# Kernel tuning notes

Hardware: AMD Instinct MI355X
Metric: run time of the kernel (lower is better)

The kernel has to match this reference:

```python
import jax, jax.numpy as jnp
import numpy as np

E = 512       # embed_dim
H = 8         # num_heads
DH = E // H   # head dim
F = 2048      # dim_feedforward
KS = 33       # NATTEN kernel_size (dilation=1)
NCLS = 1
B = 2
L = 4096      # local tokens (total seq = L + NCLS)
EPS = 1e-5


def layernorm(x, g, b):
    mu = jnp.mean(x, axis=-1, keepdims=True)
    var = jnp.mean(jnp.square(x - mu), axis=-1, keepdims=True)
    return (x - mu) * jax.lax.rsqrt(var + EPS) * g + b


def natten_1d(x, qkv_w, qkv_b, proj_w, proj_b):
    # Neighborhood attention 1D, dilation=1, non-causal, no rel-pos bias.
    b, l, e = x.shape
    qkv = x @ qkv_w.T + qkv_b                       # [b, l, 3E]
    q, k, v = jnp.split(qkv, 3, axis=-1)
    q = q.reshape(b, l, H, DH) * (DH ** -0.5)
    k = k.reshape(b, l, H, DH)
    v = v.reshape(b, l, H, DH)
    # NATTEN window: centered, shifted at edges to keep exactly KS in-bounds neighbors
    starts = jnp.clip(jnp.arange(l) - KS // 2, 0, l - KS)   # [l]
    idx = starts[:, None] + jnp.arange(KS)                  # [l, KS]
    kn = k[:, idx]                                          # [b, l, KS, H, DH]
    vn = v[:, idx]                                          # [b, l, KS, H, DH]
    attn = jnp.einsum('blhd,blkhd->bhlk', q, kn)
    attn = jax.nn.softmax(attn, axis=-1)
    out = jnp.einsum('bhlk,blkhd->blhd', attn, vn).reshape(b, l, e)
    return out @ proj_w.T + proj_b


def global_mha(q_in, kv_in, in_w, in_b, out_w, out_b):
    # torch nn.MultiheadAttention, batch_first, no masks
    bq, lq, e = q_in.shape
    lk = kv_in.shape[1]
    wq, wk, wv = jnp.split(in_w, 3, axis=0)
    bqp, bkp, bvp = jnp.split(in_b, 3, axis=0)
    q = (q_in @ wq.T + bqp).reshape(bq, lq, H, DH) * (DH ** -0.5)
    k = (kv_in @ wk.T + bkp).reshape(bq, lk, H, DH)
    v = (kv_in @ wv.T + bvp).reshape(bq, lk, H, DH)
    attn = jax.nn.softmax(jnp.einsum('bqhd,bkhd->bhqk', q, k), axis=-1)
    out = jnp.einsum('bhqk,bkhd->bqhd', attn, v).reshape(bq, lq, e)
    return out @ out_w.T + out_b


def setup_inputs() -> dict:
    key = jax.random.key(0)
    ks = jax.random.split(key, 16)
    s = 0.02
    return {
        'x': jax.random.normal(ks[0], (B, L + NCLS, E), jnp.float32),
        'ln1_g': jnp.ones((E,), jnp.float32),
        'ln1_b': jnp.zeros((E,), jnp.float32),
        'qkv_w': jax.random.normal(ks[1], (3 * E, E), jnp.float32) * s,
        'qkv_b': jnp.zeros((3 * E,), jnp.float32),
        'na_proj_w': jax.random.normal(ks[2], (E, E), jnp.float32) * s,
        'na_proj_b': jnp.zeros((E,), jnp.float32),
        'in_proj_w': jax.random.normal(ks[3], (3 * E, E), jnp.float32) * s,
        'in_proj_b': jnp.zeros((3 * E,), jnp.float32),
        'out_w': jax.random.normal(ks[4], (E, E), jnp.float32) * s,
        'out_b': jnp.zeros((E,), jnp.float32),
        'ln2_g': jnp.ones((E,), jnp.float32),
        'ln2_b': jnp.zeros((E,), jnp.float32),
        'fc1_w': jax.random.normal(ks[5], (F, E), jnp.float32) * s,
        'fc1_b': jnp.zeros((F,), jnp.float32),
        'fc2_w': jax.random.normal(ks[6], (E, F), jnp.float32) * s,
        'fc2_b': jnp.zeros((E,), jnp.float32),
    }


def reference(x, ln1_g, ln1_b, qkv_w, qkv_b, na_proj_w, na_proj_b,
              in_proj_w, in_proj_b, out_w, out_b, ln2_g, ln2_b,
              fc1_w, fc1_b, fc2_w, fc2_b):
    res = x
    xn = layernorm(x, ln1_g, ln1_b)
    x_local = natten_1d(xn[:, :-NCLS, :], qkv_w, qkv_b, na_proj_w, na_proj_b)
    tmp_key = jnp.concatenate([x_local, xn[:, -NCLS:, :]], axis=1)
    x_cls = global_mha(xn[:, -NCLS:, :], tmp_key, in_proj_w, in_proj_b, out_w, out_b)
    x = res + jnp.concatenate([x_local, x_cls], axis=1)
    res = x
    xn = layernorm(x, ln2_g, ln2_b)
    h = jax.nn.silu(xn @ fc1_w.T + fc1_b)
    return res + (h @ fc2_w.T + fc2_b)
```

## Files before the change

### kernel.cpp

```cpp
#include <hip/hip_runtime.h>
#include <hip/hip_bf16.h>
#include <cstdint>
#include <cstddef>

#define E    512
#define H    8
#define DHD  64
#define FDIM 2048
#define KS   33
#define BB   2
#define LL   4096
#define LP1  4097
#define NTOK 8194
#define NLOC 8192

typedef unsigned short ushort_t;
typedef __bf16 bf16x8_t __attribute__((ext_vector_type(8)));
typedef float  f32x4_t  __attribute__((ext_vector_type(4)));

__device__ __forceinline__ float b2f(unsigned short h) {
  union { unsigned int u; float f; } un; un.u = ((unsigned int)h) << 16; return un.f;
}
__device__ __forceinline__ unsigned short f2b(float f) {
  union { float f; unsigned int u; } un; un.f = f;
  unsigned int u = un.u;
  return (unsigned short)((u + 0x7FFFu + ((u >> 16) & 1u)) >> 16);
}

__device__ __forceinline__ void gload16(const ushort_t* g, ushort_t* l) {
  __builtin_amdgcn_global_load_lds(
      (const __attribute__((address_space(1))) void*)g,
      (__attribute__((address_space(3))) void*)l,
      16, 0, 0);
}

#define BM 128

template<int BNT, int ACT, int OUTF, int ADDRES, int INRM, int OUTRM, int PARTIAL>
__global__ __launch_bounds__(256) void gemm_bt(
    const ushort_t* __restrict__ A, const ushort_t* __restrict__ W,
    const float* __restrict__ bias, float* __restrict__ outF,
    ushort_t* __restrict__ outB, const float* __restrict__ res,
    int M, int N, int K, int klen)
{
  constexpr int NFRAG = BNT / 32;
  __shared__ ushort_t Alds[BM * 64];
  __shared__ ushort_t Blds[BNT * 64];
  const int t    = threadIdx.x;
  const int lane = t & 63;
  const int w    = t >> 6;
  const int wr   = w >> 1, wc = w & 1;
  const int bmBase = blockIdx.x * BM;
  const int bnBase = blockIdx.y * BNT;
  const int z    = blockIdx.z;
  const int kbeg = z * klen;

  f32x4_t zero = {0.f, 0.f, 0.f, 0.f};
  f32x4_t acc[4][NFRAG];
  #pragma unroll
  for (int m = 0; m < 4; ++m)
    #pragma unroll
    for (int n = 0; n < NFRAG; ++n) acc[m][n] = zero;

  const int srow = t >> 3;
  const int jsw8 = ((t & 7) ^ (srow & 7)) * 8;
  int arow[4];
  #pragma unroll
  for (int r = 0; r < 4; ++r) {
    int rr = bmBase + r * 32 + srow;
    if (INRM) rr += rr >> 12;
    else if (rr >= M) rr = M - 1;
    arow[r] = rr;
  }
  int brow[NFRAG];
  #pragma unroll
  for (int r = 0; r < NFRAG; ++r) brow[r] = bnBase + r * 32 + srow;

  const int frow = lane & 15;
  const int g    = lane >> 4;

  for (int k0 = kbeg; k0 < kbeg + klen; k0 += 64) {
    #pragma unroll
    for (int r = 0; r < 4; ++r)
      gload16(A + (size_t)arow[r] * K + k0 + jsw8, &Alds[(size_t)(r * 256 + t) * 8]);
    #pragma unroll
    for (int r = 0; r < NFRAG; ++r)
      gload16(W + (size_t)brow[r] * K + k0 + jsw8, &Blds[(size_t)(r * 256 + t) * 8]);
    __syncthreads();
    #pragma unroll
    for (int kk2 = 0; kk2 < 2; ++kk2) {
      bf16x8_t af[4], bfv[NFRAG];
      const int kosw = ((kk2 * 4 + g) ^ (frow & 7)) << 4;
      #pragma unroll
      for (int m = 0; m < 4; ++m) {
        int row = wr * 64 + m * 16 + frow;
        af[m] = *reinterpret_cast<const bf16x8_t*>((char*)Alds + row * 128 + kosw);
      }
      #pragma unroll
      for (int n = 0; n < NFRAG; ++n) {
        int row = wc * (BNT / 2) + n * 16 + frow;
        bfv[n] = *reinterpret_cast<const bf16x8_t*>((char*)Blds + row * 128 + kosw);
      }
      #pragma unroll
      for (int m = 0; m < 4; ++m)
        #pragma unroll
        for (int n = 0; n < NFRAG; ++n)
          acc[m][n] = __builtin_amdgcn_mfma_f32_16x16x32_bf16(af[m], bfv[n], acc[m][n], 0, 0, 0);
    }
    __syncthreads();
  }

  const int rbase = g * 4;
  const int cbase = frow;
  float* po = nullptr;
  if (PARTIAL) po = (z == 0) ? outF : (float*)outB;
  #pragma unroll
  for (int m = 0; m < 4; ++m) {
    #pragma unroll
    for (int r = 0; r < 4; ++r) {
      int gr = bmBase + wr * 64 + m * 16 + rbase + r;
      if (gr < M) {
        int orow = OUTRM ? gr + (gr >> 12) : gr;
        #pragma unroll
        for (int n = 0; n < NFRAG; ++n) {
          int gc = bnBase + wc * (BNT / 2) + n * 16 + cbase;
          float v = acc[m][n][r];
          if (PARTIAL) {
            po[(size_t)orow * N + gc] = v;
          } else {
            v += bias[gc];
            if (ACT == 1) v = v / (1.f + __expf(-v));
            if (ADDRES) v += res[(size_t)gr * N + gc];
            if (OUTF) outF[(size_t)orow * N + gc] = v;
            else      outB[(size_t)orow * N + gc] = f2b(v);
          }
        }
      }
    }
  }
}

__global__ __launch_bounds__(256) void fc2_reduce(
    float* __restrict__ out, const float* __restrict__ p0,
    const float* __restrict__ bias, const float* __restrict__ xa)
{
  size_t i = (size_t)blockIdx.x * 256 + threadIdx.x;
  float4 o = reinterpret_cast<const float4*>(out)[i];
  float4 a = reinterpret_cast<const float4*>(p0)[i];
  float4 x = reinterpret_cast<const float4*>(xa)[i];
  float4 bcol = reinterpret_cast<const float4*>(bias)[i & 127];
  o.x += a.x + x.x + bcol.x;
  o.y += a.y + x.y + bcol.y;
  o.z += a.z + x.z + bcol.z;
  o.w += a.w + x.w + bcol.w;
  reinterpret_cast<float4*>(out)[i] = o;
}

__global__ __launch_bounds__(256) void ln_fused1(
    const float* __restrict__ x, const float* __restrict__ g,
    const float* __restrict__ be, ushort_t* __restrict__ xn,
    ushort_t* __restrict__ tmpk)
{
  __shared__ float sh[4];
  const int row = blockIdx.x;
  const int t = threadIdx.x;
  const float* xr = x + (size_t)row * E;
  float v0 = xr[t], v1 = xr[t + 256];
  float sum = v0 + v1;
  #pragma unroll
  for (int o = 32; o; o >>= 1) sum += __shfl_xor(sum, o);
  if ((t & 63) == 0) sh[t >> 6] = sum;
  __syncthreads();
  float mean = (sh[0] + sh[1] + sh[2] + sh[3]) * (1.f / E);
  __syncthreads();
  float d0 = v0 - mean, d1 = v1 - mean;
  float vs = d0 * d0 + d1 * d1;
  #pragma unroll
  for (int o = 32; o; o >>= 1) vs += __shfl_xor(vs, o);
  if ((t & 63) == 0) sh[t >> 6] = vs;
  __syncthreads();
  float var = (sh[0] + sh[1] + sh[2] + sh[3]) * (1.f / E);
  float rstd = rsqrtf(var + 1e-5f);
  unsigned short o0 = f2b(d0 * rstd * g[t] + be[t]);
  unsigned short o1 = f2b(d1 * rstd * g[t + 256] + be[t + 256]);
  xn[(size_t)row * E + t] = o0;
  xn[(size_t)row * E + t + 256] = o1;
  if ((row % LP1) == LL) {
    tmpk[(size_t)row * E + t] = o0;
    tmpk[(size_t)row * E + t + 256] = o1;
  }
}

__global__ __launch_bounds__(256) void resid_ln2(
    const float* __restrict__ x, const ushort_t* __restrict__ tmpk,
    const float* __restrict__ xcls, const float* __restrict__ g,
    const float* __restrict__ be, float* __restrict__ xa,
    ushort_t* __restrict__ xn2)
{
  __shared__ float sh[4];
  const int row = blockIdx.x;
  const int b = row / LP1, l = row % LP1;
  const int t = threadIdx.x;
  float a0, a1;
  if (l < LL) { a0 = b2f(tmpk[(size_t)row * E + t]); a1 = b2f(tmpk[(size_t)row * E + t + 256]); }
  else        { a0 = xcls[b * E + t];                a1 = xcls[b * E + t + 256]; }
  float v0 = x[(size_t)row * E + t] + a0;
  float v1 = x[(size_t)row * E + t + 256] + a1;
  xa[(size_t)row * E + t] = v0;
  xa[(size_t)row * E + t + 256] = v1;
  float sum = v0 + v1;
  #pragma unroll
  for (int o = 32; o; o >>= 1) sum += __shfl_xor(sum, o);
  if ((t & 63) == 0) sh[t >> 6] = sum;
  __syncthreads();
  float mean = (sh[0] + sh[1] + sh[2] + sh[3]) * (1.f / E);
  __syncthreads();
  float d0 = v0 - mean, d1 = v1 - mean;
  float vs = d0 * d0 + d1 * d1;
  #pragma unroll
  for (int o = 32; o; o >>= 1) vs += __shfl_xor(vs, o);
  if ((t & 63) == 0) sh[t >> 6] = vs;
  __syncthreads();
  float var = (sh[0] + sh[1] + sh[2] + sh[3]) * (1.f / E);
  float rstd = rsqrtf(var + 1e-5f);
  xn2[(size_t)row * E + t]       = f2b(d0 * rstd * g[t] + be[t]);
  xn2[(size_t)row * E + t + 256] = f2b(d1 * rstd * g[t + 256] + be[t + 256]);
}

__global__ __launch_bounds__(256) void natten_mfma(
    const ushort_t* __restrict__ qkv, ushort_t* __restrict__ out)
{
  __shared__ ushort_t KP[4][64 * 64];
  __shared__ ushort_t VT[4][64 * 72];
  const int w    = threadIdx.x >> 6;
  const int lane = threadIdx.x & 63;
  const int task = blockIdx.x * 4 + w;
  const int h  = task & 7;
  const int qb = (task >> 3) & 127;
  const int b  = task >> 10;
  const int l0 = qb * 32;
  const int kb = l0 - 16;
  const ushort_t* base = qkv + (size_t)b * LL * (3 * E);
  ushort_t* Klds = KP[w];
  ushort_t* Vt   = VT[w];

  {
    const int rsub = lane >> 3;
    const int d0   = (lane & 7) * 8;
    #pragma unroll
    for (int i = 0; i < 8; ++i) {
      int row = i * 8 + rsub;
      int gl = kb + row; gl = gl < 0 ? 0 : (gl > LL - 1 ? LL - 1 : gl);
      bf16x8_t kv = *reinterpret_cast<const bf16x8_t*>(
          base + (size_t)gl * (3 * E) + E + h * 64 + d0);
      int ba = (row * 128 + d0 * 2) ^ ((row & 7) << 4);
      *reinterpret_cast<bf16x8_t*>((char*)Klds + ba) = kv;
    }
  }
  {
    const int a  = lane & 7;
    const int c8 = lane >> 3;
    unsigned int* Vt32 = (unsigned int*)Vt;
    #pragma unroll
    for (int i = 0; i < 4; ++i) {
      int rp = i * 8 + c8;
      int g0 = kb + rp * 2;     g0 = g0 < 0 ? 0 : (g0 > LL - 1 ? LL - 1 : g0);
      int g1 = kb + rp * 2 + 1; g1 = g1 < 0 ? 0 : (g1 > LL - 1 ? LL - 1 : g1);
      const ushort_t* v0 = base + (size_t)g0 * (3 * E) + 2 * E + h * 64 + a * 8;
      const ushort_t* v1 = base + (size_t)g1 * (3 * E) + 2 * E + h * 64 + a * 8;
      ushort4 x0 = *(const ushort4*)v0,       x1 = *(const ushort4*)v1;
      ushort4 y0 = *(const ushort4*)(v0 + 4), y1 = *(const ushort4*)(v1 + 4);
      int d = a * 8;
      Vt32[(d + 0) * 36 + rp] = (unsigned)x0.x | ((unsigned)x1.x << 16);
      Vt32[(d + 1) * 36 + rp] = (unsigned)x0.y | ((unsigned)x1.y << 16);
      Vt32[(d + 2) * 36 + rp] = (unsigned)x0.z | ((unsigned)x1.z << 16);
      Vt32[(d + 3) * 36 + rp] = (unsigned)x0.w | ((unsigned)x1.w << 16);
      Vt32[(d + 4) * 36 + rp] = (unsigned)y0.x | ((unsigned)y1.x << 16);
      Vt32[(d + 5) * 36 + rp] = (unsigned)y0.y | ((unsigned)y1.y << 16);
      Vt32[(d + 6) * 36 + rp] = (unsigned)y0.z | ((unsigned)y1.z << 16);
      Vt32[(d + 7) * 36 + rp] = (unsigned)y0.w | ((unsigned)y1.w << 16);
    }
  }

  const int p = lane & 15, g = lane >> 4;
  bf16x8_t qf[2][2];
  #pragma unroll
  for (int mt = 0; mt < 2; ++mt)
    #pragma unroll
    for (int ks = 0; ks < 2; ++ks)
      qf[mt][ks] = *reinterpret_cast<const bf16x8_t*>(
          base + (size_t)(l0 + mt * 16 + p) * (3 * E) + h * 64 + ks * 32 + g * 8);

  f32x4_t zero = {0.f, 0.f, 0.f, 0.f};
  f32x4_t accS[2][4];
  #pragma unroll
  for (int mt = 0; mt < 2; ++mt)
    #pragma unroll
    for (int nt = 0; nt < 4; ++nt) accS[mt][nt] = zero;
  #pragma unroll
  for (int ks = 0; ks < 2; ++ks) {
    bf16x8_t kf[4];
    #pragma unroll
    for (int nt = 0; nt < 4; ++nt) {
      int row = nt * 16 + p;
      int ba = (row * 128 + (ks * 32 + g * 8) * 2) ^ ((row & 7) << 4);
      kf[nt] = *reinterpret_cast<const bf16x8_t*>((char*)Klds + ba);
    }
    #pragma unroll
    for (int mt = 0; mt < 2; ++mt)
      #pragma unroll
      for (int nt = 0; nt < 4; ++nt)
        accS[mt][nt] = __builtin_amdgcn_mfma_f32_16x16x32_bf16(qf[mt][ks], kf[nt], accS[mt][nt], 0, 0, 0);
  }

  ushort_t* Plds = Klds;
  #pragma unroll
  for (int mt = 0; mt < 2; ++mt) {
    #pragma unroll
    for (int r = 0; r < 4; ++r) {
      int lq = l0 + mt * 16 + g * 4 + r;
      int st = lq - 16; st = st < 0 ? 0 : (st > LL - KS ? LL - KS : st);
      int clo = st - kb, chi = clo + 32;
      float sv[4];
      float mx = -1e30f;
      #pragma unroll
      for (int nt = 0; nt < 4; ++nt) {
        int c = nt * 16 + p;
        float s = accS[mt][nt][r] * 0.125f;
        s = (c >= clo && c <= chi) ? s : -1e30f;
        sv[nt] = s;
        mx = fmaxf(mx, s);
      }
      mx = fmaxf(mx, __shfl_xor(mx, 1));
      mx = fmaxf(mx, __shfl_xor(mx, 2));
      mx = fmaxf(mx, __shfl_xor(mx, 4));
      mx = fmaxf(mx, __shfl_xor(mx, 8));
      float sum = 0.f;
      #pragma unroll
      for (int nt = 0; nt < 4; ++nt) { float e = __expf(sv[nt] - mx); sv[nt] = e; sum += e; }
      sum += __shfl_xor(sum, 1);
      sum += __shfl_xor(sum, 2);
      sum += __shfl_xor(sum, 4);
      sum += __shfl_xor(sum, 8);
      float inv = 1.f / sum;
      int q = mt * 16 + g * 4 + r;
      #pragma unroll
      for (int nt = 0; nt < 4; ++nt)
        Plds[q * 72 + nt * 16 + p] = f2b(sv[nt] * inv);
    }
  }

  f32x4_t accO[2][4];
  #pragma unroll
  for (int mt = 0; mt < 2; ++mt)
    #pragma unroll
    for (int nt = 0; nt < 4; ++nt) accO[mt][nt] = zero;
  #pragma unroll
  for (int ks = 0; ks < 2; ++ks) {
    bf16x8_t pf[2], vf[4];
    #pragma unroll
    for (int mt = 0; mt < 2; ++mt)
      pf[mt] = *reinterpret_cast<const bf16x8_t*>(
          (char*)Plds + (mt * 16 + p) * 144 + (ks * 32 + g * 8) * 2);
    #pragma unroll
    for (int nt = 0; nt < 4; ++nt)
      vf[nt] = *reinterpret_cast<const bf16x8_t*>(
          (char*)Vt + (nt * 16 + p) * 144 + (ks * 32 + g * 8) * 2);
    #pragma unroll
    for (int mt = 0; mt < 2; ++mt)
      #pragma unroll
      for (int nt = 0; nt < 4; ++nt)
        accO[mt][nt] = __builtin_amdgcn_mfma_f32_16x16x32_bf16(pf[mt], vf[nt], accO[mt][nt], 0, 0, 0);
  }

  #pragma unroll
  for (int mt = 0; mt < 2; ++mt) {
    #pragma unroll
    for (int r = 0; r < 4; ++r) {
      int lq = l0 + mt * 16 + g * 4 + r;
      ushort_t* orow = out + ((size_t)(b * LL) + lq) * E + h * 64;
      #pragma unroll
      for (int nt = 0; nt < 4; ++nt)
        orow[nt * 16 + p] = f2b(accO[mt][nt][r]);
    }
  }
}

__global__ __launch_bounds__(256) void qcls_kernel(
    const ushort_t* __restrict__ xn, const float* __restrict__ inw,
    const float* __restrict__ inb, float* __restrict__ qcls)
{
  int i = blockIdx.x * 256 + threadIdx.x;
  int b = i >> 9, d = i & 511;
  const ushort_t* xr = xn + ((size_t)b * LP1 + LL) * E;
  const float* wr = inw + (size_t)d * E;
  float s = 0.f;
  for (int e = 0; e < E; e += 4) {
    ushort4 xv = *reinterpret_cast<const ushort4*>(xr + e);
    s += b2f(xv.x) * wr[e] + b2f(xv.y) * wr[e + 1] + b2f(xv.z) * wr[e + 2] + b2f(xv.w) * wr[e + 3];
  }
  qcls[i] = (s + inb[d]) * 0.125f;
}

__global__ __launch_bounds__(256) void gscore_kernel(
    const float* __restrict__ qcls, const ushort_t* __restrict__ kv,
    float* __restrict__ sc)
{
  const int wav = blockIdx.x * 4 + (threadIdx.x >> 6);
  if (wav >= BB * LP1) return;
  const int lane = threadIdx.x & 63;
  const int b = wav / LP1, j = wav % LP1;
  const ushort_t* kr = kv + (size_t)wav * 1024 + lane * 8;
  const float* q = qcls + b * E + lane * 8;
  ushort4 ka = *reinterpret_cast<const ushort4*>(kr);
  ushort4 kb4 = *reinterpret_cast<const ushort4*>(kr + 4);
  float s = b2f(ka.x) * q[0] + b2f(ka.y) * q[1] + b2f(ka.z) * q[2] + b2f(ka.w) * q[3]
          + b2f(kb4.x) * q[4] + b2f(kb4.y) * q[5] + b2f(kb4.z) * q[6] + b2f(kb4.w) * q[7];
  s += __shfl_xor(s, 1); s += __shfl_xor(s, 2); s += __shfl_xor(s, 4);
  if ((lane & 7) == 0) sc[((size_t)(b * 8) + (lane >> 3)) * LP1 + j] = s;
}

__global__ __launch_bounds__(256) void gsoftmax_kernel(float* __restrict__ sc)
{
  float* row = sc + (size_t)blockIdx.x * LP1;
  __shared__ float sh[4];
  const int t = threadIdx.x;
  float m = -1e30f;
  for (int i = t; i < LP1; i += 256) m = fmaxf(m, row[i]);
  #pragma unroll
  for (int o = 32; o; o >>= 1) m = fmaxf(m, __shfl_xor(m, o));
  if ((t & 63) == 0) sh[t >> 6] = m;
  __syncthreads();
  m = fmaxf(fmaxf(sh[0], sh[1]), fmaxf(sh[2], sh[3]));
  __syncthreads();
  float s = 0.f;
  for (int i = t; i < LP1; i += 256) { float e = __expf(row[i] - m); row[i] = e; s += e; }
  #pragma unroll
  for (int o = 32; o; o >>= 1) s += __shfl_xor(s, o);
  if ((t & 63) == 0) sh[t >> 6] = s;
  __syncthreads();
  float inv = 1.f / (sh[0] + sh[1] + sh[2] + sh[3]);
  for (int i = t; i < LP1; i += 256) row[i] *= inv;
}

__global__ __launch_bounds__(256) void gpv_kernel(
    const float* __restrict__ sc, const ushort_t* __restrict__ kv,
    float* __restrict__ parts)
{
  __shared__ float red[4][64];
  const int bh = blockIdx.y;
  const int b = bh >> 3, h = bh & 7;
  const int c = blockIdx.x;
  const int lane = threadIdx.x & 63, s4 = threadIdx.x >> 6;
  const int j0 = c * 512;
  const int jend = (j0 + 512 < LP1) ? j0 + 512 : LP1;
  const float* prow = sc + (size_t)bh * LP1;
  const ushort_t* vbase = kv + (size_t)b * LP1 * 1024 + 512 + h * 64 + lane;
  float acc = 0.f;
  for (int j = j0 + s4; j < jend; j += 4)
    acc += prow[j] * b2f(vbase[(size_t)j * 1024]);
  red[s4][lane] = acc;
  __syncthreads();
  if (s4 == 0)
    parts[((size_t)c * 16 + bh) * 64 + lane] = red[0][lane] + red[1][lane] + red[2][lane] + red[3][lane];
}

__global__ void gpv_reduce(const float* __restrict__ parts, float* __restrict__ oc)
{
  int i = blockIdx.x * 256 + threadIdx.x;
  if (i < BB * E) {
    float s = 0.f;
    #pragma unroll
    for (int c = 0; c < 9; ++c) s += parts[c * 1024 + i];
    oc[i] = s;
  }
}

__global__ __launch_bounds__(256) void xcls_kernel(
    const float* __restrict__ oc, const float* __restrict__ ow,
    const float* __restrict__ ob, float* __restrict__ xc)
{
  int i = blockIdx.x * 256 + threadIdx.x;
  if (i >= BB * E) return;
  int b = i >> 9, n = i & 511;
  const float* o = oc + b * E;
  const float* wr = ow + (size_t)n * E;
  float s = ob[n];
  for (int m = 0; m < E; ++m) s += o[m] * wr[m];
  xc[i] = s;
}

__global__ void cvt_all(
    const float* __restrict__ s0, ushort_t* __restrict__ d0, int n0,
    const float* __restrict__ s1, ushort_t* __restrict__ d1, int n1,
    const float* __restrict__ s2, ushort_t* __restrict__ d2, int n2,
    const float* __restrict__ s3, ushort_t* __restrict__ d3, int n3,
    const float* __restrict__ s4, ushort_t* __restrict__ d4, int n4)
{
  int i = (blockIdx.x * 256 + threadIdx.x) * 4;
  const float* s; ushort_t* d;
  if (i < n0)                { s = s0; d = d0; }
  else if ((i -= n0) < n1)   { s = s1; d = d1; }
  else if ((i -= n1) < n2)   { s = s2; d = d2; }
  else if ((i -= n2) < n3)   { s = s3; d = d3; }
  else if ((i -= n3) < n4)   { s = s4; d = d4; }
  else return;
  float4 v = *reinterpret_cast<const float4*>(s + i);
  ushort4 o;
  o.x = f2b(v.x); o.y = f2b(v.y); o.z = f2b(v.z); o.w = f2b(v.w);
  *reinterpret_cast<ushort4*>(d + i) = o;
}

extern "C" void kernel_launch(void* const* d_in, const int* in_sizes, int n_in,
                              void* d_out, int out_size, void* d_ws, size_t ws_size,
                              hipStream_t stream)
{
  const float* x      = (const float*)d_in[0];
  const float* ln1_g  = (const float*)d_in[1];
  const float* ln1_b  = (const float*)d_in[2];
  const float* qkv_w  = (const float*)d_in[3];
  const float* qkv_b  = (const float*)d_in[4];
  const float* na_w   = (const float*)d_in[5];
  const float* na_b   = (const float*)d_in[6];
  const float* in_w   = (const float*)d_in[7];
  const float* in_b   = (const float*)d_in[8];
  const float* out_w  = (const float*)d_in[9];
  const float* out_b  = (const float*)d_in[10];
  const float* ln2_g  = (const float*)d_in[11];
  const float* ln2_b  = (const float*)d_in[12];
  const float* fc1_w  = (const float*)d_in[13];
  const float* fc1_b  = (const float*)d_in[14];
  const float* fc2_w  = (const float*)d_in[15];
  const float* fc2_b  = (const float*)d_in[16];
  float* out = (float*)d_out;

  char* pws = (char*)d_ws;
  size_t off = 0;
  auto alloc = [&](size_t bytes) {
    void* r = pws + off; off = (off + bytes + 255) & ~(size_t)255; return r;
  };
  ushort_t* w_qkv = (ushort_t*)alloc((size_t)3 * E * E * 2);
  ushort_t* w_na  = (ushort_t*)alloc((size_t)E * E * 2);
  ushort_t* w_in  = (ushort_t*)alloc((size_t)3 * E * E * 2);
  ushort_t* w_fc1 = (ushort_t*)alloc((size_t)FDIM * E * 2);
  ushort_t* w_fc2 = (ushort_t*)alloc((size_t)E * FDIM * 2);
  ushort_t* xn1   = (ushort_t*)alloc((size_t)NTOK * E * 2);
  char*     bigR  = (char*)alloc((size_t)NTOK * FDIM * 2);
  ushort_t* qkvb  = (ushort_t*)bigR;
  ushort_t* natt  = (ushort_t*)(bigR + (size_t)NLOC * 3 * E * 2);
  ushort_t* kvg   = (ushort_t*)bigR;
  ushort_t* hbuf  = (ushort_t*)bigR;
  ushort_t* tmpk  = (ushort_t*)alloc((size_t)NTOK * E * 2);
  float*    sc    = (float*)alloc((size_t)BB * H * LP1 * 4);
  float*    qcls  = (float*)alloc(1024 * 4);
  float*    parts = (float*)alloc(9 * 16 * 64 * 4);
  float*    oc    = (float*)alloc(1024 * 4);
  float*    xcls  = (float*)alloc(1024 * 4);
  float*    xa    = (float*)alloc((size_t)NTOK * E * 4);
  ushort_t* xn2   = xn1;
  size_t off_before_s0 = off;
  float*    s0    = (float*)alloc((size_t)NTOK * E * 4);
  const bool can_split = (off <= ws_size);
  if (!can_split) off = off_before_s0;

  cvt_all<<<3840, 256, 0, stream>>>(
      qkv_w, w_qkv, 3 * E * E,
      na_w,  w_na,  E * E,
      in_w,  w_in,  3 * E * E,
      fc1_w, w_fc1, FDIM * E,
      fc2_w, w_fc2, E * FDIM);

  ln_fused1<<<NTOK, 256, 0, stream>>>(x, ln1_g, ln1_b, xn1, tmpk);
  qcls_kernel<<<4, 256, 0, stream>>>(xn1, in_w, in_b, qcls);
  gemm_bt<128,0,0,0,1,0,0><<<dim3(NLOC / BM, 3 * E / 128), 256, 0, stream>>>(
      xn1, w_qkv, qkv_b, nullptr, qkvb, nullptr, NLOC, 3 * E, E, E);
  natten_mfma<<<512, 256, 0, stream>>>(qkvb, natt);
  gemm_bt<128,0,0,0,0,1,0><<<dim3(NLOC / BM, E / 128), 256, 0, stream>>>(
      natt, w_na, na_b, nullptr, tmpk, nullptr, NLOC, E, E, E);
  gemm_bt<128,0,0,0,0,0,0><<<dim3((NTOK + BM - 1) / BM, 1024 / 128), 256, 0, stream>>>(
      tmpk, w_in + (size_t)E * E, in_b + E, nullptr, kvg, nullptr, NTOK, 1024, E, E);
  gscore_kernel<<<(BB * LP1 + 3) / 4, 256, 0, stream>>>(qcls, kvg, sc);
  gsoftmax_kernel<<<BB * H, 256, 0, stream>>>(sc);
  gpv_kernel<<<dim3(9, BB * H), 256, 0, stream>>>(sc, kvg, parts);
  gpv_reduce<<<4, 256, 0, stream>>>(parts, oc);
  xcls_kernel<<<4, 256, 0, stream>>>(oc, out_w, out_b, xcls);
  resid_ln2<<<NTOK, 256, 0, stream>>>(x, tmpk, xcls, ln2_g, ln2_b, xa, xn2);
  gemm_bt<128,1,0,0,0,0,0><<<dim3((NTOK + BM - 1) / BM, FDIM / 128), 256, 0, stream>>>(
      xn2, w_fc1, fc1_b, nullptr, hbuf, nullptr, NTOK, FDIM, E, E);
  if (can_split) {
    gemm_bt<64,0,0,0,0,0,1><<<dim3((NTOK + BM - 1) / BM, E / 64, 2), 256, 0, stream>>>(
        hbuf, w_fc2, fc2_b, s0, (ushort_t*)out, nullptr, NTOK, E, FDIM, FDIM / 2);
    fc2_reduce<<<(NTOK * E / 4) / 256, 256, 0, stream>>>(out, s0, fc2_b, xa);
  } else {
    gemm_bt<64,0,1,1,0,0,0><<<dim3((NTOK + BM - 1) / BM, E / 64), 256, 0, stream>>>(
        hbuf, w_fc2, fc2_b, out, nullptr, xa, NTOK, E, FDIM, FDIM);
  }
}
```

Before: 287.5 us.

## Double-buffer GEMM LDS tiles, remap blocks across XCDs, widen fc2 tiles

The GEMM kernel now keeps two LDS buffers. It prefetches the next K-tile with global_load_lds while the MFMAs for the current tile run, and drops one barrier per iteration. Launches become 1D grids, and a XCD-aware remap gives each XCD a contiguous run of tiles to improve L2 reuse of shared A/W panels. The fc2 GEMM moves from 64- to 128-wide N tiles. This doubles LDS use, which may lower occupancy, and holds both k-halves of fragments in registers.

```diff
diff --git a/kernel.cpp b/kernel.cpp
--- a/kernel.cpp
+++ b/kernel.cpp
@@ -34,6 +34,12 @@
       16, 0, 0);
 }
 
+__device__ __forceinline__ int xcd_remap(int hw, int n) {
+  int xcd = hw & 7, j = hw >> 3;
+  int q = n >> 3, r = n & 7;
+  return (xcd < r ? xcd * (q + 1) : r * (q + 1) + (xcd - r) * q) + j;
+}
+
 #define BM 128
 
 template<int BNT, int ACT, int OUTF, int ADDRES, int INRM, int OUTRM, int PARTIAL>
@@ -41,18 +47,23 @@
     const ushort_t* __restrict__ A, const ushort_t* __restrict__ W,
     const float* __restrict__ bias, float* __restrict__ outF,
     ushort_t* __restrict__ outB, const float* __restrict__ res,
-    int M, int N, int K, int klen)
+    int M, int N, int K, int klen, int ny, int nz)
 {
   constexpr int NFRAG = BNT / 32;
-  __shared__ ushort_t Alds[BM * 64];
-  __shared__ ushort_t Blds[BNT * 64];
+  __shared__ ushort_t Alds[2][BM * 64];
+  __shared__ ushort_t Blds[2][BNT * 64];
   const int t    = threadIdx.x;
   const int lane = t & 63;
   const int w    = t >> 6;
   const int wr   = w >> 1, wc = w & 1;
-  const int bmBase = blockIdx.x * BM;
-  const int bnBase = blockIdx.y * BNT;
-  const int z    = blockIdx.z;
+
+  const int Lid = xcd_remap(blockIdx.x, gridDim.x);
+  const int bx  = Lid / (ny * nz);
+  const int rem = Lid % (ny * nz);
+  const int z   = rem / ny;
+  const int by  = rem % ny;
+  const int bmBase = bx * BM;
+  const int bnBase = by * BNT;
   const int kbeg = z * klen;
 
   f32x4_t zero = {0.f, 0.f, 0.f, 0.f};
@@ -79,34 +90,44 @@
   const int frow = lane & 15;
   const int g    = lane >> 4;
 
-  for (int k0 = kbeg; k0 < kbeg + klen; k0 += 64) {
+  auto STAGE = [&](int s, int k0) {
     #pragma unroll
     for (int r = 0; r < 4; ++r)
-      gload16(A + (size_t)arow[r] * K + k0 + jsw8, &Alds[(size_t)(r * 256 + t) * 8]);
+      gload16(A + (size_t)arow[r] * K + k0 + jsw8, &Alds[s][(size_t)(r * 256 + t) * 8]);
     #pragma unroll
     for (int r = 0; r < NFRAG; ++r)
-      gload16(W + (size_t)brow[r] * K + k0 + jsw8, &Blds[(size_t)(r * 256 + t) * 8]);
-    __syncthreads();
+      gload16(W + (size_t)brow[r] * K + k0 + jsw8, &Blds[s][(size_t)(r * 256 + t) * 8]);
+  };
+
+  const int nt = klen >> 6;
+  STAGE(0, kbeg);
+  __syncthreads();
+
+  for (int it = 0; it < nt; ++it) {
+    const int cur = it & 1;
+    bf16x8_t af[2][4], bfv[2][NFRAG];
     #pragma unroll
     for (int kk2 = 0; kk2 < 2; ++kk2) {
-      bf16x8_t af[4], bfv[NFRAG];
       const int kosw = ((kk2 * 4 + g) ^ (frow & 7)) << 4;
       #pragma unroll
       for (int m = 0; m < 4; ++m) {
         int row = wr * 64 + m * 16 + frow;
-        af[m] = *reinterpret_cast<const bf16x8_t*>((char*)Alds + row * 128 + kosw);
+        af[kk2][m] = *reinterpret_cast<const bf16x8_t*>((char*)Alds[cur] + row * 128 + kosw);
       }
       #pragma unroll
       for (int n = 0; n < NFRAG; ++n) {
         int row = wc * (BNT / 2) + n * 16 + frow;
-        bfv[n] = *reinterpret_cast<const bf16x8_t*>((char*)Blds + row * 128 + kosw);
+        bfv[kk2][n] = *reinterpret_cast<const bf16x8_t*>((char*)Blds[cur] + row * 128 + kosw);
       }
+    }
+    if (it + 1 < nt) STAGE(cur ^ 1, kbeg + (it + 1) * 64);
+    #pragma unroll
+    for (int kk2 = 0; kk2 < 2; ++kk2)
       #pragma unroll
       for (int m = 0; m < 4; ++m)
         #pragma unroll
         for (int n = 0; n < NFRAG; ++n)
-          acc[m][n] = __builtin_amdgcn_mfma_f32_16x16x32_bf16(af[m], bfv[n], acc[m][n], 0, 0, 0);
-    }
+          acc[m][n] = __builtin_amdgcn_mfma_f32_16x16x32_bf16(af[kk2][m], bfv[kk2][n], acc[m][n], 0, 0, 0);
     __syncthreads();
   }
 
@@ -572,27 +593,27 @@
 
   ln_fused1<<<NTOK, 256, 0, stream>>>(x, ln1_g, ln1_b, xn1, tmpk);
   qcls_kernel<<<4, 256, 0, stream>>>(xn1, in_w, in_b, qcls);
-  gemm_bt<128,0,0,0,1,0,0><<<dim3(NLOC / BM, 3 * E / 128), 256, 0, stream>>>(
-      xn1, w_qkv, qkv_b, nullptr, qkvb, nullptr, NLOC, 3 * E, E, E);
+  gemm_bt<128,0,0,0,1,0,0><<<64 * 12, 256, 0, stream>>>(
+      xn1, w_qkv, qkv_b, nullptr, qkvb, nullptr, NLOC, 3 * E, E, E, 12, 1);
   natten_mfma<<<512, 256, 0, stream>>>(qkvb, natt);
-  gemm_bt<128,0,0,0,0,1,0><<<dim3(NLOC / BM, E / 128), 256, 0, stream>>>(
-      natt, w_na, na_b, nullptr, tmpk, nullptr, NLOC, E, E, E);
-  gemm_bt<128,0,0,0,0,0,0><<<dim3((NTOK + BM - 1) / BM, 1024 / 128), 256, 0, stream>>>(
-      tmpk, w_in + (size_t)E * E, in_b + E, nullptr, kvg, nullptr, NTOK, 1024, E, E);
+  gemm_bt<128,0,0,0,0,1,0><<<64 * 4, 256, 0, stream>>>(
+      natt, w_na, na_b, nullptr, tmpk, nullptr, NLOC, E, E, E, 4, 1);
+  gemm_bt<128,0,0,0,0,0,0><<<65 * 8, 256, 0, stream>>>(
+      tmpk, w_in + (size_t)E * E, in_b + E, nullptr, kvg, nullptr, NTOK, 1024, E, E, 8, 1);
   gscore_kernel<<<(BB * LP1 + 3) / 4, 256, 0, stream>>>(qcls, kvg, sc);
   gsoftmax_kernel<<<BB * H, 256, 0, stream>>>(sc);
   gpv_kernel<<<dim3(9, BB * H), 256, 0, stream>>>(sc, kvg, parts);
   gpv_reduce<<<4, 256, 0, stream>>>(parts, oc);
   xcls_kernel<<<4, 256, 0, stream>>>(oc, out_w, out_b, xcls);
   resid_ln2<<<NTOK, 256, 0, stream>>>(x, tmpk, xcls, ln2_g, ln2_b, xa, xn2);
-  gemm_bt<128,1,0,0,0,0,0><<<dim3((NTOK + BM - 1) / BM, FDIM / 128), 256, 0, stream>>>(
-      xn2, w_fc1, fc1_b, nullptr, hbuf, nullptr, NTOK, FDIM, E, E);
+  gemm_bt<128,1,0,0,0,0,0><<<65 * 16, 256, 0, stream>>>(
+      xn2, w_fc1, fc1_b, nullptr, hbuf, nullptr, NTOK, FDIM, E, E, 16, 1);
   if (can_split) {
-    gemm_bt<64,0,0,0,0,0,1><<<dim3((NTOK + BM - 1) / BM, E / 64, 2), 256, 0, stream>>>(
-        hbuf, w_fc2, fc2_b, s0, (ushort_t*)out, nullptr, NTOK, E, FDIM, FDIM / 2);
+    gemm_bt<128,0,0,0,0,0,1><<<65 * 4 * 2, 256, 0, stream>>>(
+        hbuf, w_fc2, fc2_b, s0, (ushort_t*)out, nullptr, NTOK, E, FDIM, FDIM / 2, 4, 2);
     fc2_reduce<<<(NTOK * E / 4) / 256, 256, 0, stream>>>(out, s0, fc2_b, xa);
   } else {
-    gemm_bt<64,0,1,1,0,0,0><<<dim3((NTOK + BM - 1) / BM, E / 64), 256, 0, stream>>>(
-        hbuf, w_fc2, fc2_b, out, nullptr, xa, NTOK, E, FDIM, FDIM);
-  }
-}
+    gemm_bt<128,0,1,1,0,0,0><<<65 * 4, 256, 0, stream>>>(
+        hbuf, w_fc2, fc2_b, out, nullptr, xa, NTOK, E, FDIM, FDIM, 4, 1);
+  }
+}
```

Measured after the change: 280.7 us. -2.4%, faster.
